# Kernel tuning notes

Measured on AMD Instinct MI355X. Metric: run time of the kernel, lower is better.

The kernel has to match this reference:

```python
import jax, jax.numpy as jnp
import numpy as np

DEVICE_DIM, SERVER_DIM, HIDDEN, HEAD_HIDDEN = 14, 3, 64, 128
B, N_DEV = 16384, 63
N_NODES = N_DEV + 1


def setup_inputs() -> dict:
    key = jax.random.key(0)
    ks = jax.random.split(key, 16)
    device_obs = jax.random.normal(ks[0], (B, N_DEV, DEVICE_DIM), dtype=jnp.float32)
    server_obs = jax.random.normal(ks[1], (B, SERVER_DIM), dtype=jnp.float32)
    # binary adjacency with self-loops (as built by _dense_adjacency_from_edge_index)
    rand = jax.random.uniform(ks[2], (B, N_NODES, N_NODES))
    adjacency = jnp.clip((rand < 0.3).astype(jnp.float32) + jnp.eye(N_NODES, dtype=jnp.float32), 0.0, 1.0)

    def lin(k, fan_in, fan_out):
        w = jax.random.normal(k, (fan_in, fan_out), dtype=jnp.float32) / np.sqrt(fan_in)
        return w

    return {
        'device_obs': device_obs,
        'server_obs': server_obs,
        'adjacency': adjacency,
        'W_dev': lin(ks[3], DEVICE_DIM, HIDDEN), 'b_dev': jnp.zeros((HIDDEN,), jnp.float32),
        'W_srv': lin(ks[4], SERVER_DIM, HIDDEN), 'b_srv': jnp.zeros((HIDDEN,), jnp.float32),
        'W1': lin(ks[5], HIDDEN, HIDDEN), 'b1': jnp.zeros((HIDDEN,), jnp.float32),
        'W2': lin(ks[6], HIDDEN, HIDDEN), 'b2': jnp.zeros((HIDDEN,), jnp.float32),
        'W3': lin(ks[7], HIDDEN, HIDDEN), 'b3': jnp.zeros((HIDDEN,), jnp.float32),
        'Wf1': lin(ks[8], HIDDEN * 3, HEAD_HIDDEN), 'bf1': jnp.zeros((HEAD_HIDDEN,), jnp.float32),
        'Wf2': lin(ks[9], HEAD_HIDDEN, 1), 'bf2': jnp.zeros((1,), jnp.float32),
    }


def _dense_gcn(x, adj_norm, W, b):
    # normalized adjacency matmul then linear: [B,N,N]@[B,N,H] -> [B,N,H]
    return jnp.einsum('bnm,bmh->bnh', adj_norm, x) @ W + b


def reference(device_obs, server_obs, adjacency,
              W_dev, b_dev, W_srv, b_srv,
              W1, b1, W2, b2, W3, b3,
              Wf1, bf1, Wf2, bf2):
    # node encoding
    device_emb = jax.nn.relu(device_obs @ W_dev + b_dev)            # [B,Nd,H]
    server_emb = jax.nn.relu(server_obs @ W_srv + b_srv)[:, None]   # [B,1,H]
    x = jnp.concatenate([device_emb, server_emb], axis=1)           # [B,N,H]

    # symmetric degree normalization D^-1/2 A D^-1/2 (degree clamped to >=1)
    degree = adjacency.sum(axis=-1)
    d_inv_sqrt = jnp.clip(degree, 1.0, None) ** -0.5
    adj_norm = d_inv_sqrt[:, :, None] * adjacency * d_inv_sqrt[:, None, :]

    h = jax.nn.relu(_dense_gcn(x, adj_norm, W1, b1))
    h = jax.nn.relu(_dense_gcn(h, adj_norm, W2, b2))
    h = jax.nn.relu(_dense_gcn(h, adj_norm, W3, b3))

    # head
    server_hidden = h[:, -1]                  # [B,H]
    device_hidden = h[:, :-1]                 # [B,Nd,H]
    dev_mean = device_hidden.mean(axis=1)     # [B,H]
    n = device_hidden.shape[1]
    shared_srv = jnp.broadcast_to(server_hidden[:, None], (h.shape[0], n, HIDDEN))
    shared_mean = jnp.broadcast_to(dev_mean[:, None], (h.shape[0], n, HIDDEN))
    critic_in = jnp.concatenate([device_hidden, shared_mean, shared_srv], axis=-1)  # [B,Nd,3H]
    out = jax.nn.relu(critic_in @ Wf1 + bf1) @ Wf2 + bf2
    return out[..., 0]  # [B,Nd]
```

## Files before the change

kernel.cpp:

```cpp
#include <hip/hip_runtime.h>
#include <stdint.h>

typedef __attribute__((ext_vector_type(8))) __bf16 bf16x8;
typedef __attribute__((ext_vector_type(4))) float f32x4;
typedef __attribute__((ext_vector_type(2))) float f32x2;
typedef __attribute__((ext_vector_type(4))) unsigned uint4v;
typedef __attribute__((ext_vector_type(2))) unsigned uint2v;

union U4 { uint4v u; bf16x8 b; };

#define WS_WDEV_H 0
#define WS_WDEV_L 4096
#define WS_W1_H   8192
#define WS_W1_L   16384
#define WS_W2_H   24576
#define WS_W2_L   32768
#define WS_W3_H   40960
#define WS_W3_L   49152
#define WS_WA_H   57344
#define WS_WA_L   73728
#define WS_WF_H   90112
#define WS_WF_L   122880

__device__ __forceinline__ unsigned short f2bf(float f){
  union { float f; unsigned u; } v; v.f = f;
  unsigned r = v.u + 0x7fffu + ((v.u >> 16) & 1u);
  return (unsigned short)(r >> 16);
}
__device__ __forceinline__ float bf2f(unsigned short h){
  union { unsigned u; float f; } v; v.u = ((unsigned)h) << 16; return v.f;
}
__device__ __forceinline__ void split2(float x, unsigned short& hi, unsigned short& lo){
  hi = f2bf(x);
  lo = f2bf(x - bf2f(hi));
}
__device__ __forceinline__ f32x4 mfma16(const U4& a, const U4& b, f32x4 c){
  return __builtin_amdgcn_mfma_f32_16x16x32_bf16(a.b, b.b, c, 0, 0, 0);
}

__device__ __forceinline__ unsigned rnu(unsigned u){
  return u + 0x7fffu + ((u >> 16) & 1u);
}
__device__ __forceinline__ void split_pair(float x0, float x1, unsigned& hi2, unsigned& lo2){
  unsigned r0 = rnu(__float_as_uint(x0)), r1 = rnu(__float_as_uint(x1));
  float l0 = x0 - __uint_as_float(r0 & 0xffff0000u);
  float l1 = x1 - __uint_as_float(r1 & 0xffff0000u);
  hi2 = __builtin_amdgcn_perm(r1, r0, 0x07060302u);
  unsigned s0 = rnu(__float_as_uint(l0)), s1 = rnu(__float_as_uint(l1));
  lo2 = __builtin_amdgcn_perm(s1, s0, 0x07060302u);
}
__device__ __forceinline__ unsigned pack_hl(float z){
  unsigned r = rnu(__float_as_uint(z));
  float lf = z - __uint_as_float(r & 0xffff0000u);
  unsigned s = rnu(__float_as_uint(lf));
  return __builtin_amdgcn_perm(s, r, 0x07060302u);
}

extern "C" __global__ void prep_weights(const float* __restrict__ Wdev,
                                        const float* __restrict__ W1,
                                        const float* __restrict__ W2,
                                        const float* __restrict__ W3,
                                        const float* __restrict__ Wf1,
                                        char* __restrict__ ws)
{
  unsigned short* WdevH = (unsigned short*)(ws + WS_WDEV_H);
  unsigned short* WdevL = (unsigned short*)(ws + WS_WDEV_L);
  unsigned short* WH[3] = {(unsigned short*)(ws+WS_W1_H),(unsigned short*)(ws+WS_W2_H),(unsigned short*)(ws+WS_W3_H)};
  unsigned short* WL[3] = {(unsigned short*)(ws+WS_W1_L),(unsigned short*)(ws+WS_W2_L),(unsigned short*)(ws+WS_W3_L)};
  unsigned short* WaH = (unsigned short*)(ws + WS_WA_H);
  unsigned short* WaL = (unsigned short*)(ws + WS_WA_L);
  unsigned short* WfH = (unsigned short*)(ws + WS_WF_H);
  unsigned short* WfL = (unsigned short*)(ws + WS_WF_L);
  const int total = 2048 + 3*4096 + 8192 + 16384;
  for (int idx = blockIdx.x*256 + threadIdx.x; idx < total; idx += gridDim.x*256){
    if (idx < 2048){
      int tt = idx;
      int frag = tt >> 9, within = tt & 511, lane = within >> 3, j = within & 7;
      int nt = frag & 3;
      int k = ((lane>>4)<<3) + j;
      int n = (nt<<4) + (lane & 15);
      float v = (k < 14) ? Wdev[k*64 + n] : 0.f;
      unsigned short h,l; split2(v,h,l); WdevH[tt]=h; WdevL[tt]=l;
    } else if (idx < 2048 + 3*4096){
      int tt = idx - 2048; int Li = tt / 4096; int r = tt - Li*4096;
      int frag = r >> 9, within = r & 511, lane = within >> 3, j = within & 7;
      int ks = frag >> 2, nt = frag & 3;
      int k = (ks<<5) + ((lane>>4)<<3) + j;
      int n = (nt<<4) + (lane & 15);
      const float* W = (Li==0) ? W1 : ((Li==1) ? W2 : W3);
      float v = W[k*64 + n];
      unsigned short h,l; split2(v,h,l); WH[Li][r]=h; WL[Li][r]=l;
    } else if (idx < 2048 + 3*4096 + 8192){
      int r = idx - (2048 + 3*4096);
      int frag = r >> 9, within = r & 511, lane = within >> 3, j = within & 7;
      int ks = frag >> 3, nt = frag & 7;
      int k = (ks<<5) + ((lane>>4)<<3) + j;
      int n = (nt<<4) + (lane & 15);
      float v = Wf1[k*128 + n];
      unsigned short h,l; split2(v,h,l); WaH[r]=h; WaL[r]=l;
    } else {
      int r = idx - (2048 + 3*4096 + 8192);
      int frag = r >> 9, within = r & 511, lane = within >> 3, j = within & 7;
      int ks = frag >> 3, nt = frag & 7;
      int k = (ks<<5) + ((lane>>4)<<3) + j;
      int n = (nt<<4) + (lane & 15);
      float v = Wf1[(64 + k)*128 + n];
      unsigned short h,l; split2(v,h,l); WfH[r]=h; WfL[r]=l;
    }
  }
}

extern "C" __global__ __launch_bounds__(256, 6)
void pgcn_fused(const float* __restrict__ dobs, const float* __restrict__ sobs,
                const float* __restrict__ adj,
                const float* __restrict__ bdev,
                const float* __restrict__ Wsrv, const float* __restrict__ bsrv,
                const float* __restrict__ b1, const float* __restrict__ b2,
                const float* __restrict__ b3,
                const float* __restrict__ bf1, const float* __restrict__ Wf2,
                const float* __restrict__ bf2,
                const char* __restrict__ ws, float* __restrict__ out)
{
  __shared__ __align__(16) unsigned long long lds_Abits[64];
  __shared__ __align__(16) float    lds_d[64];
  __shared__ __align__(16) unsigned lds_R1[4096];
  __shared__ __align__(16) float    lds_mp[256];
  __shared__ __align__(16) float    lds_srv[64];
  __shared__ __align__(16) float    lds_s1[128];
  __shared__ __align__(16) unsigned short lds_Vh[128];
  __shared__ __align__(16) unsigned short lds_Vl[128];

  const int t = threadIdx.x;
  const int w = t >> 6;
  const int lane = t & 63;
  const int quad = lane >> 4;
  const int c = lane & 15;
  const long item = blockIdx.x;

  {
    const f32x4* src = (const f32x4*)(adj + item*4096 + ((t>>2)<<6) + ((t&3)<<4));
    unsigned bits = 0;
    for (int i = 0; i < 4; ++i){
      f32x4 v = src[i];
      unsigned b = (v.x != 0.f) | (((unsigned)(v.y != 0.f))<<1)
                 | (((unsigned)(v.z != 0.f))<<2) | (((unsigned)(v.w != 0.f))<<3);
      bits |= b << (i<<2);
    }
    ((unsigned short*)lds_Abits)[t] = (unsigned short)bits;
  }

  unsigned ahi[4] = {0,0,0,0}, alo[4] = {0,0,0,0};
  {
    int m = (w<<4) + c;
    if (quad < 2 && m < 63){
      const float* rp = dobs + item*882 + m*14 + (quad<<3);
      float e[8];
      f32x2 p0 = *(const f32x2*)(rp);
      f32x2 p1 = *(const f32x2*)(rp+2);
      f32x2 p2 = *(const f32x2*)(rp+4);
      e[0]=p0.x; e[1]=p0.y; e[2]=p1.x; e[3]=p1.y; e[4]=p2.x; e[5]=p2.y;
      if (quad == 0){
        f32x2 p3 = *(const f32x2*)(rp+6);
        e[6]=p3.x; e[7]=p3.y;
      } else {
        e[6]=0.f; e[7]=0.f;
      }
      for (int d0 = 0; d0 < 4; ++d0)
        split_pair(e[2*d0], e[2*d0+1], ahi[d0], alo[d0]);
    }
  }
  __syncthreads();

  if (t < 64){
    unsigned long long mk = lds_Abits[t];
    int deg = __popcll(mk);
    lds_d[t] = 1.0f / sqrtf((float)(deg < 1 ? 1 : deg));
  }
  __syncthreads();

  f32x4 d4v = *(const f32x4*)&lds_d[(w<<4) + (quad<<2)];
  const float dd[4] = {d4v.x, d4v.y, d4v.z, d4v.w};

  U4 af0, af1;
  {
    unsigned long long mk = lds_Abits[(w<<4) + c];
    unsigned blo = ((unsigned)mk) >> (quad<<3);
    unsigned bhi = ((unsigned)(mk >> 32)) >> (quad<<3);
    for (int r = 0; r < 4; ++r){
      unsigned e0 = 0u - ((blo >> (2*r)) & 1u);
      unsigned o0 = 0u - ((blo >> (2*r+1)) & 1u);
      af0.u[r] = (e0 & 0x3f80u) | (o0 & 0x3f800000u);
      unsigned e1 = 0u - ((bhi >> (2*r)) & 1u);
      unsigned o1 = 0u - ((bhi >> (2*r+1)) & 1u);
      af1.u[r] = (e1 & 0x3f80u) | (o1 & 0x3f800000u);
    }
  }

  const int laneCy = c + ((w&1)<<5) + ((quad>>1)<<4);
  const int j0 = (quad&1)<<2;
  const int kspY = w>>1;
  unsigned short* Yhi = (unsigned short*)lds_R1;
  unsigned short* Ylo = ((unsigned short*)lds_R1) + 4096;

  float hcur[4][4];

  {
    U4 a_h, a_l;
    a_h.u = uint4v{ahi[0],ahi[1],ahi[2],ahi[3]};
    a_l.u = uint4v{alo[0],alo[1],alo[2],alo[3]};
    const uint4v* WdH = (const uint4v*)(ws + WS_WDEV_H);
    const uint4v* WdL = (const uint4v*)(ws + WS_WDEV_L);
    float srvv4[4];
    if (w == 3 && quad == 3){
      float s0 = sobs[item*3+0], s1v = sobs[item*3+1], s2v = sobs[item*3+2];
      for (int nt = 0; nt < 4; ++nt){
        int col = c + (nt<<4);
        float v = s0*Wsrv[col] + s1v*Wsrv[64+col] + s2v*Wsrv[128+col] + bsrv[col];
        srvv4[nt] = fmaxf(v, 0.f);
      }
    }
    for (int nt = 0; nt < 4; ++nt){
      U4 wh, wl;
      wh.u = WdH[(nt<<6) + lane];
      wl.u = WdL[(nt<<6) + lane];
      f32x4 g = {0.f,0.f,0.f,0.f};
      g = mfma16(a_h, wh, g);
      g = mfma16(a_h, wl, g);
      g = mfma16(a_l, wh, g);
      float bb = bdev[c + (nt<<4)];
      float y[4];
      for (int r = 0; r < 4; ++r) y[r] = fmaxf(g[r] + bb, 0.f);
      if (w == 3 && quad == 3) y[3] = srvv4[nt];
      for (int r = 0; r < 4; ++r) y[r] *= dd[r];
      unsigned h01, l01, h23, l23;
      split_pair(y[0], y[1], h01, l01);
      split_pair(y[2], y[3], h23, l23);
      int base = ((((kspY<<2) + nt) << 6) + laneCy)*8 + j0;
      *(uint2v*)&Yhi[base] = uint2v{ h01, h23 };
      *(uint2v*)&Ylo[base] = uint2v{ l01, l23 };
    }
  }
  __syncthreads();

  const uint4v* WH_tab[3] = {(const uint4v*)(ws+WS_W1_H),(const uint4v*)(ws+WS_W2_H),(const uint4v*)(ws+WS_W3_H)};
  const uint4v* WL_tab[3] = {(const uint4v*)(ws+WS_W1_L),(const uint4v*)(ws+WS_W2_L),(const uint4v*)(ws+WS_W3_L)};
  const float* bias_tab[3] = {b1, b2, b3};

  unsigned* zbuf = lds_R1 + (w<<10);
  const int piL = (lane>>2) | ((lane&3)<<4);
  const int s0L = (piL>>2) & 1;

  for (int L = 0; L < 3; ++L){
    const uint4v* Yhi4 = (const uint4v*)lds_R1;
    const uint4v* Ylo4 = ((const uint4v*)lds_R1) + 512;
    f32x4 zacc[4];
    for (int nt = 0; nt < 4; ++nt){
      f32x4 g = {0.f,0.f,0.f,0.f};
      U4 yh, yl;
      yh.u = Yhi4[(0*4+nt)*64 + lane]; yl.u = Ylo4[(0*4+nt)*64 + lane];
      g = mfma16(af0, yh, g); g = mfma16(af0, yl, g);
      yh.u = Yhi4[(1*4+nt)*64 + lane]; yl.u = Ylo4[(1*4+nt)*64 + lane];
      g = mfma16(af1, yh, g); g = mfma16(af1, yl, g);
      zacc[nt] = g;
    }
    __syncthreads();

    for (int nt = 0; nt < 4; ++nt){
      int ks = nt >> 1;
      int lcBase = (quad<<2) + ((((nt&1)<<1) + (c>>3)) << 4);
      int e = c & 7;
      for (int r = 0; r < 4; ++r){
        unsigned pk = pack_hl(zacc[nt][r] * dd[r]);
        int lane_c = lcBase + r;
        int pi = (lane_c>>2) | ((lane_c&3)<<4);
        int sel = ((e>>2) ^ (pi>>2)) & 1;
        zbuf[(ks<<9) + (pi<<3) + (sel<<2) + (e&3)] = pk;
      }
    }
    __threadfence_block();
    U4 zh[2], zl[2];
    for (int ks = 0; ks < 2; ++ks){
      uint4v qa = *(const uint4v*)&zbuf[(ks<<9) + (piL<<3) + (s0L<<2)];
      uint4v qb = *(const uint4v*)&zbuf[(ks<<9) + (piL<<3) + ((1-s0L)<<2)];
      zh[ks].u = uint4v{ (qa.y<<16)|(qa.x&0xffffu), (qa.w<<16)|(qa.z&0xffffu),
                         (qb.y<<16)|(qb.x&0xffffu), (qb.w<<16)|(qb.z&0xffffu) };
      zl[ks].u = uint4v{ (qa.y&0xffff0000u)|(qa.x>>16), (qa.w&0xffff0000u)|(qa.z>>16),
                         (qb.y&0xffff0000u)|(qb.x>>16), (qb.w&0xffff0000u)|(qb.z>>16) };
    }

    const uint4v* WHp = WH_tab[L];
    const uint4v* WLp = WL_tab[L];
    const float* bp = bias_tab[L];
    for (int nt = 0; nt < 4; ++nt){
      f32x4 g = {0.f,0.f,0.f,0.f};
      for (int ks = 0; ks < 2; ++ks){
        U4 wh, wl;
        wh.u = WHp[((ks<<2)+nt)*64 + lane];
        wl.u = WLp[((ks<<2)+nt)*64 + lane];
        g = mfma16(zh[ks], wh, g);
        g = mfma16(zh[ks], wl, g);
        g = mfma16(zl[ks], wh, g);
      }
      float bb = bp[c + (nt<<4)];
      for (int r = 0; r < 4; ++r) hcur[nt][r] = fmaxf(g[r] + bb, 0.f);
    }
    __syncthreads();

    if (L < 2){
      for (int nt = 0; nt < 4; ++nt){
        unsigned h01, l01, h23, l23;
        split_pair(hcur[nt][0]*dd[0], hcur[nt][1]*dd[1], h01, l01);
        split_pair(hcur[nt][2]*dd[2], hcur[nt][3]*dd[3], h23, l23);
        int base = ((((kspY<<2) + nt) << 6) + laneCy)*8 + j0;
        *(uint2v*)&Yhi[base] = uint2v{ h01, h23 };
        *(uint2v*)&Ylo[base] = uint2v{ l01, l23 };
      }
      __syncthreads();
    }
  }

  {
    bool isSrvLane = (w == 3) && (quad == 3);
    float cs[4];
    for (int nt = 0; nt < 4; ++nt){
      float s = hcur[nt][0] + hcur[nt][1] + hcur[nt][2] + hcur[nt][3];
      if (isSrvLane){ s -= hcur[nt][3]; lds_srv[c + (nt<<4)] = hcur[nt][3]; }
      s += __shfl_xor(s, 16);
      s += __shfl_xor(s, 32);
      cs[nt] = s;
    }
    if (quad == 0)
      for (int nt = 0; nt < 4; ++nt) lds_mp[(w<<6) + c + (nt<<4)] = cs[nt];
  }
  for (int nt = 0; nt < 4; ++nt){
    int ks = nt >> 1;
    int lcBase = (quad<<2) + ((((nt&1)<<1) + (c>>3)) << 4);
    int e = c & 7;
    for (int r = 0; r < 4; ++r){
      unsigned pk = pack_hl(hcur[nt][r]);
      int lane_c = lcBase + r;
      int pi = (lane_c>>2) | ((lane_c&3)<<4);
      int sel = ((e>>2) ^ (pi>>2)) & 1;
      zbuf[(ks<<9) + (pi<<3) + (sel<<2) + (e&3)] = pk;
    }
  }
  __syncthreads();

  if (t < 64){
    float mv = (lds_mp[t] + lds_mp[64+t] + lds_mp[128+t] + lds_mp[192+t]) * (1.0f/63.0f);
    unsigned short h,l; split2(mv,h,l);
    lds_Vh[t]=h; lds_Vl[t]=l;
  } else if (t < 128){
    float sv = lds_srv[t-64];
    unsigned short h,l; split2(sv,h,l);
    lds_Vh[t]=h; lds_Vl[t]=l;
  }
  __syncthreads();

  U4 hh[2], hl[2];
  for (int ks = 0; ks < 2; ++ks){
    uint4v qa = *(const uint4v*)&zbuf[(ks<<9) + (piL<<3) + (s0L<<2)];
    uint4v qb = *(const uint4v*)&zbuf[(ks<<9) + (piL<<3) + ((1-s0L)<<2)];
    hh[ks].u = uint4v{ (qa.y<<16)|(qa.x&0xffffu), (qa.w<<16)|(qa.z&0xffffu),
                       (qb.y<<16)|(qb.x&0xffffu), (qb.w<<16)|(qb.z&0xffffu) };
    hl[ks].u = uint4v{ (qa.y&0xffff0000u)|(qa.x>>16), (qa.w&0xffff0000u)|(qa.z>>16),
                       (qb.y&0xffff0000u)|(qb.x>>16), (qb.w&0xffff0000u)|(qb.z>>16) };
  }

  {
    const uint4v* WfH = (const uint4v*)(ws + WS_WF_H);
    const uint4v* WfL = (const uint4v*)(ws + WS_WF_L);
    f32x4 sacc0 = {0.f,0.f,0.f,0.f}, sacc1 = {0.f,0.f,0.f,0.f};
    for (int ks = 0; ks < 4; ++ks){
      U4 vh, vl;
      vh.u = *(const uint4v*)((const char*)lds_Vh + (ks<<6) + (quad<<4));
      vl.u = *(const uint4v*)((const char*)lds_Vl + (ks<<6) + (quad<<4));
      if (c != 0){ vh.u = uint4v{0,0,0,0}; vl.u = uint4v{0,0,0,0}; }
      int nt0 = (w<<1);
      U4 wh, wl;
      wh.u = WfH[((ks<<3)+nt0)*64 + lane];
      wl.u = WfL[((ks<<3)+nt0)*64 + lane];
      sacc0 = mfma16(vh, wh, sacc0);
      sacc0 = mfma16(vh, wl, sacc0);
      sacc0 = mfma16(vl, wh, sacc0);
      wh.u = WfH[((ks<<3)+nt0+1)*64 + lane];
      wl.u = WfL[((ks<<3)+nt0+1)*64 + lane];
      sacc1 = mfma16(vh, wh, sacc1);
      sacc1 = mfma16(vh, wl, sacc1);
      sacc1 = mfma16(vl, wh, sacc1);
    }
    if (quad == 0){
      int col0 = c + (w<<5);
      lds_s1[col0]      = sacc0[0] + bf1[col0];
      lds_s1[col0 + 16] = sacc1[0] + bf1[col0 + 16];
    }
  }
  __syncthreads();

  const uint4v* WaH = (const uint4v*)(ws + WS_WA_H);
  const uint4v* WaL = (const uint4v*)(ws + WS_WA_L);
  float outacc[4] = {0.f,0.f,0.f,0.f};
  for (int nt = 0; nt < 8; ++nt){
    f32x4 g = {0.f,0.f,0.f,0.f};
    for (int ks = 0; ks < 2; ++ks){
      U4 wh, wl;
      wh.u = WaH[((ks<<3)+nt)*64 + lane];
      wl.u = WaL[((ks<<3)+nt)*64 + lane];
      g = mfma16(hh[ks], wh, g);
      g = mfma16(hh[ks], wl, g);
      g = mfma16(hl[ks], wh, g);
    }
    int col = c + (nt<<4);
    float sv = lds_s1[col];
    float w2 = Wf2[col];
    for (int r = 0; r < 4; ++r){
      float zz = fmaxf(g[r] + sv, 0.f);
      outacc[r] += zz * w2;
    }
  }
  {
    float bb = bf2[0];
    for (int r = 0; r < 4; ++r){
      float v = outacc[r];
      v += __shfl_xor(v, 1); v += __shfl_xor(v, 2);
      v += __shfl_xor(v, 4); v += __shfl_xor(v, 8);
      if (c == 0){
        int row = (w<<4) + (quad<<2) + r;
        if (row < 63) out[item*63 + row] = v + bb;
      }
    }
  }
}

extern "C" void kernel_launch(void* const* d_in, const int* in_sizes, int n_in,
                              void* d_out, int out_size, void* d_ws, size_t ws_size,
                              hipStream_t stream)
{
  const float* dobs = (const float*)d_in[0];
  const float* sobs = (const float*)d_in[1];
  const float* adj  = (const float*)d_in[2];
  const float* Wdev = (const float*)d_in[3];
  const float* bdev = (const float*)d_in[4];
  const float* Wsrv = (const float*)d_in[5];
  const float* bsrv = (const float*)d_in[6];
  const float* W1   = (const float*)d_in[7];
  const float* b1   = (const float*)d_in[8];
  const float* W2   = (const float*)d_in[9];
  const float* b2   = (const float*)d_in[10];
  const float* W3   = (const float*)d_in[11];
  const float* b3   = (const float*)d_in[12];
  const float* Wf1  = (const float*)d_in[13];
  const float* bf1  = (const float*)d_in[14];
  const float* Wf2  = (const float*)d_in[15];
  const float* bf2  = (const float*)d_in[16];
  float* out = (float*)d_out;
  char* ws = (char*)d_ws;
  int nb = in_sizes[1] / 3;

  prep_weights<<<dim3(160), dim3(256), 0, stream>>>(Wdev, W1, W2, W3, Wf1, ws);
  pgcn_fused<<<dim3(nb), dim3(256), 0, stream>>>(dobs, sobs, adj, bdev, Wsrv, bsrv,
                                                 b1, b2, b3, bf1, Wf2, bf2, ws, out);
}
```

Baseline: 635.4 us.

## Transpose aggregation MFMA and use padded row-major LDS layout for Y and Z

Reworks the adjacency aggregation so the feature tile becomes the A operand and the adjacency bits the B operand, computing the transposed product. Y and Z are now stored in a padded row-major LDS buffer with a 72-element row stride. Z can therefore be written with plain packed stores and read back with single vector loads, instead of going through the swizzled hi/lo pack and unpack shuffle. LDS use grows slightly, which may affect occupancy, and the padding is meant to limit bank conflicts.

Result: no change. 630.2 us (-0.8%).

```diff
diff --git a/kernel.cpp b/kernel.cpp
--- a/kernel.cpp
+++ b/kernel.cpp
@@ -121,9 +121,9 @@
                 const float* __restrict__ bf2,
                 const char* __restrict__ ws, float* __restrict__ out)
 {
+  __shared__ __align__(16) unsigned short     lds_Yr[9216];
   __shared__ __align__(16) unsigned long long lds_Abits[64];
   __shared__ __align__(16) float    lds_d[64];
-  __shared__ __align__(16) unsigned lds_R1[4096];
   __shared__ __align__(16) float    lds_mp[256];
   __shared__ __align__(16) float    lds_srv[64];
   __shared__ __align__(16) float    lds_s1[128];
@@ -136,6 +136,7 @@
   const int quad = lane >> 4;
   const int c = lane & 15;
   const long item = blockIdx.x;
+  char* Yb = (char*)lds_Yr;
 
   {
     const f32x4* src = (const f32x4*)(adj + item*4096 + ((t>>2)<<6) + ((t&3)<<4));
@@ -180,27 +181,25 @@
 
   f32x4 d4v = *(const f32x4*)&lds_d[(w<<4) + (quad<<2)];
   const float dd[4] = {d4v.x, d4v.y, d4v.z, d4v.w};
-
-  U4 af0, af1;
+  const float ddc = lds_d[(w<<4) + c];
+
+  U4 atk[2];
   {
     unsigned long long mk = lds_Abits[(w<<4) + c];
-    unsigned blo = ((unsigned)mk) >> (quad<<3);
-    unsigned bhi = ((unsigned)(mk >> 32)) >> (quad<<3);
-    for (int r = 0; r < 4; ++r){
-      unsigned e0 = 0u - ((blo >> (2*r)) & 1u);
-      unsigned o0 = 0u - ((blo >> (2*r+1)) & 1u);
-      af0.u[r] = (e0 & 0x3f80u) | (o0 & 0x3f800000u);
-      unsigned e1 = 0u - ((bhi >> (2*r)) & 1u);
-      unsigned o1 = 0u - ((bhi >> (2*r+1)) & 1u);
-      af1.u[r] = (e1 & 0x3f80u) | (o1 & 0x3f800000u);
-    }
-  }
-
-  const int laneCy = c + ((w&1)<<5) + ((quad>>1)<<4);
-  const int j0 = (quad&1)<<2;
-  const int kspY = w>>1;
-  unsigned short* Yhi = (unsigned short*)lds_R1;
-  unsigned short* Ylo = ((unsigned short*)lds_R1) + 4096;
+    for (int ks = 0; ks < 2; ++ks){
+      unsigned byt = (unsigned)(mk >> ((ks<<5) + (quad<<3))) & 0xffu;
+      for (int r = 0; r < 4; ++r){
+        unsigned e = 0u - ((byt >> (2*r)) & 1u);
+        unsigned o = 0u - ((byt >> (2*r+1)) & 1u);
+        atk[ks].u[r] = (e & 0x3f80u) | (o & 0x3f800000u);
+      }
+    }
+  }
+
+  const int ybw = (c*72 + (w<<4) + (quad<<2)) << 1;
+  const int yrd = (c*72 + (quad<<3)) << 1;
+  const int zbw = (((w<<4)+c)*72 + (quad<<2)) << 1;
+  const int zrd = (((w<<4)+c)*72 + (quad<<3)) << 1;
 
   float hcur[4][4];
 
@@ -235,9 +234,8 @@
       unsigned h01, l01, h23, l23;
       split_pair(y[0], y[1], h01, l01);
       split_pair(y[2], y[3], h23, l23);
-      int base = ((((kspY<<2) + nt) << 6) + laneCy)*8 + j0;
-      *(uint2v*)&Yhi[base] = uint2v{ h01, h23 };
-      *(uint2v*)&Ylo[base] = uint2v{ l01, l23 };
+      *(uint2v*)(Yb + ybw + 2304*nt)        = uint2v{ h01, h23 };
+      *(uint2v*)(Yb + ybw + 2304*nt + 9216) = uint2v{ l01, l23 };
     }
   }
   __syncthreads();
@@ -246,46 +244,33 @@
   const uint4v* WL_tab[3] = {(const uint4v*)(ws+WS_W1_L),(const uint4v*)(ws+WS_W2_L),(const uint4v*)(ws+WS_W3_L)};
   const float* bias_tab[3] = {b1, b2, b3};
 
-  unsigned* zbuf = lds_R1 + (w<<10);
-  const int piL = (lane>>2) | ((lane&3)<<4);
-  const int s0L = (piL>>2) & 1;
-
   for (int L = 0; L < 3; ++L){
-    const uint4v* Yhi4 = (const uint4v*)lds_R1;
-    const uint4v* Ylo4 = ((const uint4v*)lds_R1) + 512;
     f32x4 zacc[4];
-    for (int nt = 0; nt < 4; ++nt){
+    for (int mt = 0; mt < 4; ++mt){
       f32x4 g = {0.f,0.f,0.f,0.f};
-      U4 yh, yl;
-      yh.u = Yhi4[(0*4+nt)*64 + lane]; yl.u = Ylo4[(0*4+nt)*64 + lane];
-      g = mfma16(af0, yh, g); g = mfma16(af0, yl, g);
-      yh.u = Yhi4[(1*4+nt)*64 + lane]; yl.u = Ylo4[(1*4+nt)*64 + lane];
-      g = mfma16(af1, yh, g); g = mfma16(af1, yl, g);
-      zacc[nt] = g;
+      for (int ks = 0; ks < 2; ++ks){
+        U4 yh, yl;
+        yh.u = *(const uint4v*)(Yb + yrd + 2304*mt + 64*ks);
+        yl.u = *(const uint4v*)(Yb + yrd + 2304*mt + 64*ks + 9216);
+        g = mfma16(yh, atk[ks], g);
+        g = mfma16(yl, atk[ks], g);
+      }
+      zacc[mt] = g;
     }
     __syncthreads();
 
-    for (int nt = 0; nt < 4; ++nt){
-      int ks = nt >> 1;
-      int lcBase = (quad<<2) + ((((nt&1)<<1) + (c>>3)) << 4);
-      int e = c & 7;
-      for (int r = 0; r < 4; ++r){
-        unsigned pk = pack_hl(zacc[nt][r] * dd[r]);
-        int lane_c = lcBase + r;
-        int pi = (lane_c>>2) | ((lane_c&3)<<4);
-        int sel = ((e>>2) ^ (pi>>2)) & 1;
-        zbuf[(ks<<9) + (pi<<3) + (sel<<2) + (e&3)] = pk;
-      }
+    for (int mt = 0; mt < 4; ++mt){
+      unsigned h01, l01, h23, l23;
+      split_pair(zacc[mt][0]*ddc, zacc[mt][1]*ddc, h01, l01);
+      split_pair(zacc[mt][2]*ddc, zacc[mt][3]*ddc, h23, l23);
+      *(uint2v*)(Yb + zbw + 32*mt)        = uint2v{ h01, h23 };
+      *(uint2v*)(Yb + zbw + 32*mt + 9216) = uint2v{ l01, l23 };
     }
     __threadfence_block();
     U4 zh[2], zl[2];
     for (int ks = 0; ks < 2; ++ks){
-      uint4v qa = *(const uint4v*)&zbuf[(ks<<9) + (piL<<3) + (s0L<<2)];
-      uint4v qb = *(const uint4v*)&zbuf[(ks<<9) + (piL<<3) + ((1-s0L)<<2)];
-      zh[ks].u = uint4v{ (qa.y<<16)|(qa.x&0xffffu), (qa.w<<16)|(qa.z&0xffffu),
-                         (qb.y<<16)|(qb.x&0xffffu), (qb.w<<16)|(qb.z&0xffffu) };
-      zl[ks].u = uint4v{ (qa.y&0xffff0000u)|(qa.x>>16), (qa.w&0xffff0000u)|(qa.z>>16),
-                         (qb.y&0xffff0000u)|(qb.x>>16), (qb.w&0xffff0000u)|(qb.z>>16) };
+      zh[ks].u = *(const uint4v*)(Yb + zrd + 64*ks);
+      zl[ks].u = *(const uint4v*)(Yb + zrd + 64*ks + 9216);
     }
 
     const uint4v* WHp = WH_tab[L];
@@ -311,13 +296,16 @@
         unsigned h01, l01, h23, l23;
         split_pair(hcur[nt][0]*dd[0], hcur[nt][1]*dd[1], h01, l01);
         split_pair(hcur[nt][2]*dd[2], hcur[nt][3]*dd[3], h23, l23);
-        int base = ((((kspY<<2) + nt) << 6) + laneCy)*8 + j0;
-        *(uint2v*)&Yhi[base] = uint2v{ h01, h23 };
-        *(uint2v*)&Ylo[base] = uint2v{ l01, l23 };
+        *(uint2v*)(Yb + ybw + 2304*nt)        = uint2v{ h01, h23 };
+        *(uint2v*)(Yb + ybw + 2304*nt + 9216) = uint2v{ l01, l23 };
       }
       __syncthreads();
     }
   }
+
+  unsigned* zbuf = (unsigned*)Yb + (w<<10);
+  const int piL = (lane>>2) | ((lane&3)<<4);
+  const int s0L = (piL>>2) & 1;
 
   {
     bool isSrvLane = (w == 3) && (quad == 3);
```
